# Optimization experiments

Hardware: AMD Instinct MI355X
Metric: run time of the kernel (lower is better)

## Reference

```python
import jax, jax.numpy as jnp
import numpy as np


def setup_inputs() -> dict:
    key = jax.random.key(0)
    ks = jax.random.split(key, 8)
    B, N, M, H = 8192, 2048, 2048, 10
    return {
        "X": jax.random.normal(ks[0], (B, N), dtype=jnp.float32),
        "weight": jax.random.normal(ks[1], (N, M), dtype=jnp.float32),
        "W1": jax.random.normal(ks[2], (3, H), dtype=jnp.float32) * 0.5,
        "b1": jax.random.normal(ks[3], (H,), dtype=jnp.float32) * 0.1,
        "W2": jax.random.normal(ks[4], (H, H), dtype=jnp.float32) * 0.3,
        "b2": jax.random.normal(ks[5], (H,), dtype=jnp.float32) * 0.1,
        "W3": jax.random.normal(ks[6], (H, 1), dtype=jnp.float32) * 0.3,
        "b3": jax.random.normal(ks[7], (1,), dtype=jnp.float32) * 0.1,
    }


def reference(X, weight, W1, b1, W2, b2, W3, b3):
    # NCA local rule, vectorized over all (i, j) cells.
    # 'forward'  = mean of column j excluding row i  (leave-one-out col mean)
    # 'backward' = mean of row i excluding column j  (leave-one-out row mean)
    n, m = weight.shape
    col_sum = jnp.sum(weight, axis=0, keepdims=True)            # [1, m]
    row_sum = jnp.sum(weight, axis=1, keepdims=True)            # [n, 1]
    fwd_mean = (col_sum - weight) / jnp.float32(n - 1)          # [n, m]
    bwd_mean = (row_sum - weight) / jnp.float32(m - 1)          # [n, m]
    feats = jnp.stack([weight, fwd_mean, bwd_mean], axis=-1)    # [n, m, 3]
    # tiny 3 -> 10 -> 10 -> 1 MLP applied per cell
    h = jax.nn.relu(feats @ W1 + b1)                            # [n, m, 10]
    h = jax.nn.relu(h @ W2 + b2)                                # [n, m, 10]
    updates = (h @ W3 + b3)[..., 0]                             # [n, m]
    new_weight = weight + updates
    # forward: softmax(X @ W)
    return jax.nn.softmax(X @ new_weight, axis=-1)
```

## Files before the change

### kernel.cpp

```cpp
#include <hip/hip_runtime.h>
#include <hip/hip_bf16.h>


typedef int int4v __attribute__((ext_vector_type(4)));
typedef int int16v __attribute__((ext_vector_type(16)));

#define GK 2048
#define NROWS 2048
#define MCOLS 2048
#define NCHUNK 16

#define CS_BLOCKS 128
#define RS_BLOCKS 2048
__global__ __launch_bounds__(256) void pre_kernel(
    const float* __restrict__ X, const float* __restrict__ W,
    signed char* __restrict__ X1, signed char* __restrict__ X2,
    float* __restrict__ sx1,
    float* __restrict__ part, float* __restrict__ rowS) {
  const int bid = blockIdx.x;
  const int tid = threadIdx.x;

  if (bid < CS_BLOCKS) {
    int chunk = bid >> 3;
    int j = (bid & 7) * 256 + tid;
    int i0 = chunk * (NROWS / NCHUNK);
    float s = 0.f;
    for (int i = i0; i < i0 + NROWS / NCHUNK; ++i) s += W[(size_t)i * MCOLS + j];
    part[(size_t)chunk * MCOLS + j] = s;
    return;
  }
  if (bid < CS_BLOCKS + RS_BLOCKS) {
    int row = bid - CS_BLOCKS;
    const float4* p = (const float4*)(W + (size_t)row * MCOLS);
    float4 a = p[tid];
    float4 b = p[tid + 256];
    float v = (a.x + a.y) + (a.z + a.w) + (b.x + b.y) + (b.z + b.w);
    __shared__ float red[256];
    red[tid] = v;
    __syncthreads();
    for (int s = 128; s > 0; s >>= 1) {
      if (tid < s) red[tid] += red[tid + s];
      __syncthreads();
    }
    if (tid == 0) rowS[row] = red[0];
    return;
  }
  {
    int row = bid - CS_BLOCKS - RS_BLOCKS;
    const float4* xr = (const float4*)(X + (size_t)row * GK);
    float4 a = xr[tid * 2];
    float4 b = xr[tid * 2 + 1];
    float xs[8] = {a.x, a.y, a.z, a.w, b.x, b.y, b.z, b.w};
    float am = 0.f;
#pragma unroll
    for (int i = 0; i < 8; ++i) am = fmaxf(am, fabsf(xs[i]));
    const int lane = tid & 63, wv = tid >> 6;
#pragma unroll
    for (int off = 32; off > 0; off >>= 1)
      am = fmaxf(am, __shfl_xor(am, off));
    __shared__ float wred[4];
    if (lane == 0) wred[wv] = am;
    __syncthreads();
    float amax = fmaxf(fmaxf(wred[0], wred[1]), fmaxf(wred[2], wred[3]));
    float s1 = amax * (1.0f / 127.0f);
    float inv = 127.0f / amax;
    int q1[8], q2[8];
#pragma unroll
    for (int i = 0; i < 8; ++i) {
      q1[i] = (int)rintf(xs[i] * inv);
      float r = xs[i] - (float)q1[i] * s1;
      q2[i] = (int)rintf(r * (254.0f * inv));
    }
    unsigned lo1 = (q1[0] & 255) | ((q1[1] & 255) << 8) | ((q1[2] & 255) << 16) | ((q1[3] & 255) << 24);
    unsigned hi1 = (q1[4] & 255) | ((q1[5] & 255) << 8) | ((q1[6] & 255) << 16) | ((q1[7] & 255) << 24);
    unsigned lo2 = (q2[0] & 255) | ((q2[1] & 255) << 8) | ((q2[2] & 255) << 16) | ((q2[3] & 255) << 24);
    unsigned hi2 = (q2[4] & 255) | ((q2[5] & 255) << 8) | ((q2[6] & 255) << 16) | ((q2[7] & 255) << 24);
    ((uint2*)(X1 + (size_t)row * GK))[tid] = make_uint2(lo1, hi1);
    ((uint2*)(X2 + (size_t)row * GK))[tid] = make_uint2(lo2, hi2);
    if (tid == 0) sx1[row] = s1;
  }
}

__global__ __launch_bounds__(256) void nca_update_kernel(
    const float* __restrict__ W, const float* __restrict__ part,
    const float* __restrict__ rowS,
    const float* __restrict__ W1, const float* __restrict__ b1,
    const float* __restrict__ W2, const float* __restrict__ b2,
    const float* __restrict__ W3, const float* __restrict__ b3,
    float* __restrict__ Wt) {
  __shared__ float sW1[30], sb1[10], sW2[100], sb2[10], sW3[10], sb3;
  __shared__ float sColS[32];
  __shared__ float cred[NCHUNK][33];
  __shared__ float Tf[32][33];
  const int tid = threadIdx.x;
  const int i0 = blockIdx.y * 32;
  const int j0 = blockIdx.x * 32;

  if (tid < 30) sW1[tid] = W1[tid];
  if (tid < 10) { sb1[tid] = b1[tid]; sb2[tid] = b2[tid]; sW3[tid] = W3[tid]; }
  if (tid >= 32 && tid < 132) sW2[tid - 32] = W2[tid - 32];
  if (tid == 0) sb3 = b3[0];

  {
    int ch = tid >> 5;
    int jl = tid & 31;
    cred[ch][jl]     = part[(size_t)ch * MCOLS + j0 + jl];
    cred[ch + 8][jl] = part[(size_t)(ch + 8) * MCOLS + j0 + jl];
  }
  __syncthreads();
  if (tid < 32) {
    float s = 0.f;
#pragma unroll
    for (int c = 0; c < NCHUNK; ++c) s += cred[c][tid];
    sColS[tid] = s;
  }
  __syncthreads();

  const int r = tid >> 5;
  const int c = tid & 31;

  float w[4], fwd[4], bwd[4];
#pragma unroll
  for (int cell = 0; cell < 4; ++cell) {
    int il = r + 8 * cell;
    float wv = W[(size_t)(i0 + il) * MCOLS + j0 + c];
    w[cell] = wv;
    fwd[cell] = (sColS[c] - wv) * (1.0f / (float)(NROWS - 1));
    bwd[cell] = (rowS[i0 + il] - wv) * (1.0f / (float)(MCOLS - 1));
  }

  float h1[4][10];
#pragma unroll
  for (int o = 0; o < 10; ++o) {
    float w1a = sW1[o], w1b = sW1[10 + o], w1c = sW1[20 + o], bb = sb1[o];
#pragma unroll
    for (int cell = 0; cell < 4; ++cell) {
      float v = fmaf(w[cell], w1a, fmaf(fwd[cell], w1b, fmaf(bwd[cell], w1c, bb)));
      h1[cell][o] = fmaxf(v, 0.f);
    }
  }
  float u[4] = {sb3, sb3, sb3, sb3};
#pragma unroll
  for (int o = 0; o < 10; ++o) {
    float h2[4];
    float bb = sb2[o];
#pragma unroll
    for (int cell = 0; cell < 4; ++cell) h2[cell] = bb;
#pragma unroll
    for (int p = 0; p < 10; ++p) {
      float wv = sW2[p * 10 + o];
#pragma unroll
      for (int cell = 0; cell < 4; ++cell) h2[cell] = fmaf(h1[cell][p], wv, h2[cell]);
    }
    float w3 = sW3[o];
#pragma unroll
    for (int cell = 0; cell < 4; ++cell) u[cell] = fmaf(fmaxf(h2[cell], 0.f), w3, u[cell]);
  }

#pragma unroll
  for (int cell = 0; cell < 4; ++cell) {
    int il = r + 8 * cell;
    Tf[il][c] = w[cell] + u[cell];
  }
  __syncthreads();

  {
    int r2 = tid >> 4;
    int ic = (tid & 15) * 2;
#pragma unroll
    for (int half = 0; half < 2; ++half) {
      int jl = r2 + 16 * half;
      float2 v = make_float2(Tf[ic][jl], Tf[ic + 1][jl]);
      *(float2*)(&Wt[(size_t)(j0 + jl) * NROWS + i0 + ic]) = v;
    }
  }
}

__global__ __launch_bounds__(256) void bquant_kernel(
    const float* __restrict__ Wt, signed char* __restrict__ B1,
    signed char* __restrict__ B2, float* __restrict__ sw1) {
  const int row = blockIdx.x;
  const int tid = threadIdx.x;
  const float4* wr = (const float4*)(Wt + (size_t)row * GK);
  float4 a = wr[tid * 2];
  float4 b = wr[tid * 2 + 1];
  float xs[8] = {a.x, a.y, a.z, a.w, b.x, b.y, b.z, b.w};
  float am = 0.f;
#pragma unroll
  for (int i = 0; i < 8; ++i) am = fmaxf(am, fabsf(xs[i]));
  const int lane = tid & 63, wv = tid >> 6;
#pragma unroll
  for (int off = 32; off > 0; off >>= 1)
    am = fmaxf(am, __shfl_xor(am, off));
  __shared__ float wred[4];
  if (lane == 0) wred[wv] = am;
  __syncthreads();
  float amax = fmaxf(fmaxf(wred[0], wred[1]), fmaxf(wred[2], wred[3]));
  float s1 = amax * (1.0f / 127.0f);
  float inv = 127.0f / amax;
  int q1[8], q2[8];
#pragma unroll
  for (int i = 0; i < 8; ++i) {
    q1[i] = (int)rintf(xs[i] * inv);
    float r = xs[i] - (float)q1[i] * s1;
    q2[i] = (int)rintf(r * (254.0f * inv));
  }
  unsigned lo1 = (q1[0] & 255) | ((q1[1] & 255) << 8) | ((q1[2] & 255) << 16) | ((q1[3] & 255) << 24);
  unsigned hi1 = (q1[4] & 255) | ((q1[5] & 255) << 8) | ((q1[6] & 255) << 16) | ((q1[7] & 255) << 24);
  unsigned lo2 = (q2[0] & 255) | ((q2[1] & 255) << 8) | ((q2[2] & 255) << 16) | ((q2[3] & 255) << 24);
  unsigned hi2 = (q2[4] & 255) | ((q2[5] & 255) << 8) | ((q2[6] & 255) << 16) | ((q2[7] & 255) << 24);
  ((uint2*)(B1 + (size_t)row * GK))[tid] = make_uint2(lo1, hi1);
  ((uint2*)(B2 + (size_t)row * GK))[tid] = make_uint2(lo2, hi2);
  if (tid == 0) sw1[row] = s1;
}

#define BM 256
#define BN 128
#define BK 64
#define NT (GK / BK)
#define BUFSZ 49152

__device__ __forceinline__ void glds16(const signed char* g, char* l) {
  __builtin_amdgcn_global_load_lds(
      (const __attribute__((address_space(1))) void*)g,
      (__attribute__((address_space(3))) void*)l, 16, 0, 0);
}

#define QUAD(mi, ni)                                                           \
  {                                                                            \
    acc_h[mi][ni] = __builtin_amdgcn_mfma_i32_32x32x32_i8(                     \
        a1f[mi][0], b1f[ni][0], acc_h[mi][ni], 0, 0, 0);                       \
    acc_c[mi][ni] = __builtin_amdgcn_mfma_i32_32x32x32_i8(                     \
        a1f[mi][0], b2f[ni][0], acc_c[mi][ni], 0, 0, 0);                       \
    acc_c[mi][ni] = __builtin_amdgcn_mfma_i32_32x32x32_i8(                     \
        a2f[mi][0], b1f[ni][0], acc_c[mi][ni], 0, 0, 0);                       \
    acc_h[mi][ni] = __builtin_amdgcn_mfma_i32_32x32x32_i8(                     \
        a1f[mi][1], b1f[ni][1], acc_h[mi][ni], 0, 0, 0);                       \
    acc_c[mi][ni] = __builtin_amdgcn_mfma_i32_32x32x32_i8(                     \
        a1f[mi][1], b2f[ni][1], acc_c[mi][ni], 0, 0, 0);                       \
    acc_c[mi][ni] = __builtin_amdgcn_mfma_i32_32x32x32_i8(                     \
        a2f[mi][1], b1f[ni][1], acc_c[mi][ni], 0, 0, 0);                       \
  }

__global__ __launch_bounds__(512, 2) void gemm_kernel(
    const signed char* __restrict__ X1, const signed char* __restrict__ X2,
    const signed char* __restrict__ B1, const signed char* __restrict__ B2,
    const float* __restrict__ sw1, float* __restrict__ C) {
  __shared__ __align__(16) char sL[3 * BUFSZ];

  const int tid = threadIdx.x;
  const int lane = tid & 63;
  const int wave = tid >> 6;
  const int wr = wave >> 1;
  const int wc = wave & 1;

  const int bx = blockIdx.x;
  const int by = blockIdx.y;

  const signed char* A1g = X1 + (size_t)(by * BM) * GK;
  const signed char* A2g = X2 + (size_t)(by * BM) * GK;
  const signed char* B1g = B1 + (size_t)(bx * BN) * GK;
  const signed char* B2g = B2 + (size_t)(bx * BN) * GK;

  const int srow = lane >> 2;
  const int schk = (lane & 3) ^ ((lane >> 3) & 3);
  const size_t qoff = (size_t)(wave * 16 + srow) * GK + schk * 16;
  const int wds = wave * 1024;

  const int rl = lane & 15;
  const int bhalf = (lane >> 4) & 1;
  const int kck = lane >> 5;
  int aoff[2][2], boff[2][2];
#pragma unroll
  for (int mi = 0; mi < 2; ++mi)
#pragma unroll
    for (int ks = 0; ks < 2; ++ks) {
      int c = 2 * ks + kck;
      int slot = 4 * rl + (c ^ ((rl >> 1) & 3));
      aoff[mi][ks] = (wr * 4 + mi * 2 + bhalf) * 1024 + slot * 16;
      boff[mi][ks] = 32768 + (wc * 4 + mi * 2 + bhalf) * 1024 + slot * 16;
    }

  int16v acc_h[2][2], acc_c[2][2];
#pragma unroll
  for (int i = 0; i < 2; ++i)
#pragma unroll
    for (int j = 0; j < 2; ++j)
#pragma unroll
      for (int e = 0; e < 16; ++e) { acc_h[i][j][e] = 0; acc_c[i][j][e] = 0; }

#pragma unroll
  for (int t = 0; t < 2; ++t) {
    char* wb = sL + t * BUFSZ;
    const size_t k0 = (size_t)t * BK;
    glds16(A1g + qoff + k0, wb + wds);
    glds16(A1g + qoff + (size_t)128 * GK + k0, wb + 8192 + wds);
    glds16(A2g + qoff + k0, wb + 16384 + wds);
    glds16(A2g + qoff + (size_t)128 * GK + k0, wb + 24576 + wds);
    glds16(B1g + qoff + k0, wb + 32768 + wds);
    glds16(B2g + qoff + k0, wb + 40960 + wds);
  }

  const char* sbuf = sL;
  char* wbuf = sL + 2 * BUFSZ;

  int4v a1f[2][2], a2f[2][2], b1f[2][2], b2f[2][2];

#pragma unroll 1
  for (int kt = 0; kt < NT; ++kt) {
    if (kt + 1 < NT) asm volatile("s_waitcnt vmcnt(6)" ::: "memory");
    else             asm volatile("s_waitcnt vmcnt(0)" ::: "memory");
    __builtin_amdgcn_s_barrier();
    asm volatile("" ::: "memory");

    const size_t k2 = (size_t)(kt + 2) * BK;
    const bool pf = (kt + 2 < NT);

#pragma unroll
    for (int ks = 0; ks < 2; ++ks) {
      a1f[0][ks] = *(const int4v*)(sbuf + aoff[0][ks]);
      a2f[0][ks] = *(const int4v*)(sbuf + aoff[0][ks] + 16384);
      b1f[0][ks] = *(const int4v*)(sbuf + boff[0][ks]);
      b2f[0][ks] = *(const int4v*)(sbuf + boff[0][ks] + 8192);
    }
    if (pf) {
      glds16(A1g + qoff + k2, wbuf + wds);
      glds16(A1g + qoff + (size_t)128 * GK + k2, wbuf + 8192 + wds);
    }
#pragma unroll
    for (int ks = 0; ks < 2; ++ks) {
      b1f[1][ks] = *(const int4v*)(sbuf + boff[1][ks]);
      b2f[1][ks] = *(const int4v*)(sbuf + boff[1][ks] + 8192);
    }
    if (pf) {
      glds16(A2g + qoff + k2, wbuf + 16384 + wds);
      glds16(A2g + qoff + (size_t)128 * GK + k2, wbuf + 24576 + wds);
    }
#pragma unroll
    for (int ks = 0; ks < 2; ++ks) {
      a1f[1][ks] = *(const int4v*)(sbuf + aoff[1][ks]);
      a2f[1][ks] = *(const int4v*)(sbuf + aoff[1][ks] + 16384);
    }
    if (pf) {
      glds16(B1g + qoff + k2, wbuf + 32768 + wds);
      glds16(B2g + qoff + k2, wbuf + 40960 + wds);
    }

    __builtin_amdgcn_s_setprio(1);
    QUAD(0, 0);
    QUAD(0, 1);
    QUAD(1, 1);
    QUAD(1, 0);
    __builtin_amdgcn_s_setprio(0);

    sbuf += BUFSZ; if (sbuf == sL + 3 * BUFSZ) sbuf = sL;
    wbuf += BUFSZ; if (wbuf == sL + 3 * BUFSZ) wbuf = sL;
  }

  const int ecol = lane & 31;
  const int erow = 4 * (lane >> 5);
#pragma unroll
  for (int ni = 0; ni < 2; ++ni) {
    int col = bx * BN + wc * 64 + ni * 32 + ecol;
    float sw = sw1[col];
#pragma unroll
    for (int mi = 0; mi < 2; ++mi) {
#pragma unroll
      for (int reg = 0; reg < 16; ++reg) {
        int row = by * BM + wr * 64 + mi * 32 + (reg & 3) + 8 * (reg >> 2) + erow;
        float v = (float)acc_h[mi][ni][reg] + (float)acc_c[mi][ni][reg] * (1.0f / 254.0f);
        C[(size_t)row * MCOLS + col] = v * sw;
      }
    }
  }
}

__global__ __launch_bounds__(256) void softmax_kernel(
    float* __restrict__ C, const float* __restrict__ sx1) {
  const int lane = threadIdx.x & 63;
  const int wv = threadIdx.x >> 6;
  const int row = blockIdx.x * 4 + wv;
  const float sx = sx1[row];
  float4* p = (float4*)(C + (size_t)row * MCOLS);

  float4 v[8];
#pragma unroll
  for (int j = 0; j < 8; ++j) {
    v[j] = p[j * 64 + lane];
    v[j].x *= sx; v[j].y *= sx; v[j].z *= sx; v[j].w *= sx;
  }

  float vmax = -3.4e38f;
#pragma unroll
  for (int j = 0; j < 8; ++j)
    vmax = fmaxf(vmax, fmaxf(fmaxf(v[j].x, v[j].y), fmaxf(v[j].z, v[j].w)));
#pragma unroll
  for (int off = 32; off > 0; off >>= 1)
    vmax = fmaxf(vmax, __shfl_xor(vmax, off));

  float sum = 0.f;
#pragma unroll
  for (int j = 0; j < 8; ++j) {
    v[j].x = __expf(v[j].x - vmax);
    v[j].y = __expf(v[j].y - vmax);
    v[j].z = __expf(v[j].z - vmax);
    v[j].w = __expf(v[j].w - vmax);
    sum += (v[j].x + v[j].y) + (v[j].z + v[j].w);
  }
#pragma unroll
  for (int off = 32; off > 0; off >>= 1)
    sum += __shfl_xor(sum, off);
  float inv = 1.0f / sum;

#pragma unroll
  for (int j = 0; j < 8; ++j) {
    v[j].x *= inv; v[j].y *= inv; v[j].z *= inv; v[j].w *= inv;
    p[j * 64 + lane] = v[j];
  }
}

extern "C" void kernel_launch(void* const* d_in, const int* in_sizes, int n_in,
                              void* d_out, int out_size, void* d_ws, size_t ws_size,
                              hipStream_t stream) {
  const float* X      = (const float*)d_in[0];
  const float* weight = (const float*)d_in[1];
  const float* W1     = (const float*)d_in[2];
  const float* b1     = (const float*)d_in[3];
  const float* W2     = (const float*)d_in[4];
  const float* b2     = (const float*)d_in[5];
  const float* W3     = (const float*)d_in[6];
  const float* b3     = (const float*)d_in[7];
  float* out = (float*)d_out;

  const int N = 2048, M = 2048;
  const int Bdim = in_sizes[0] / N;

  float* rowS = (float*)d_ws;
  float* part = rowS + 2048;
  float* sx1  = part + NCHUNK * 2048;
  float* sw1  = sx1 + 8192;
  float* Wt   = sw1 + 2048;
  signed char* X1 = (signed char*)(Wt + (size_t)M * N);
  signed char* X2 = X1 + (size_t)Bdim * N;
  signed char* B1q = X2 + (size_t)Bdim * N;
  signed char* B2q = B1q + (size_t)M * N;

  pre_kernel<<<CS_BLOCKS + RS_BLOCKS + Bdim, 256, 0, stream>>>(
      X, weight, X1, X2, sx1, part, rowS);

  nca_update_kernel<<<dim3(M / 32, N / 32), 256, 0, stream>>>(
      weight, part, rowS, W1, b1, W2, b2, W3, b3, Wt);

  bquant_kernel<<<M, 256, 0, stream>>>(Wt, B1q, B2q, sw1);

  gemm_kernel<<<dim3(M / BN, Bdim / BM), 512, 0, stream>>>(
      X1, X2, B1q, B2q, sw1, out);

  softmax_kernel<<<Bdim / 4, 256, 0, stream>>>(out, sx1);
}
```

Measured before the change: 297.4 us.

## Split MFMA block into halves gated by explicit LDS waitcnts to overlap reads

Replaces the compiler-generated LDS fragment loads with inline-asm ds_read_b128 and reorders them so all B fragments and the first A row load first. Waits with lgkmcnt(4) and runs the first half of the MFMAs (mi=0) while the mi=1 A fragments are still in flight, then waits for the rest before the second half. Sched barriers pin this order. The aim is to hide LDS read latency behind matrix work. The risk is that hand-placed waitcnts have to match the exact instruction count, since inline asm hides these loads from the compiler's dependency tracking.

```diff
diff --git a/kernel.cpp b/kernel.cpp
--- a/kernel.cpp
+++ b/kernel.cpp
@@ -226,20 +226,40 @@
       (__attribute__((address_space(3))) void*)l, 16, 0, 0);
 }
 
-#define QUAD(mi, ni)                                                           \
+__device__ __forceinline__ int4v ds_read128(const char* p) {
+  int4v r;
+  asm volatile("ds_read_b128 %0, %1"
+               : "=v"(r)
+               : "v"((const __attribute__((address_space(3))) char*)p));
+  return r;
+}
+
+#define PAIR(mi)                                                               \
   {                                                                            \
-    acc_h[mi][ni] = __builtin_amdgcn_mfma_i32_32x32x32_i8(                     \
-        a1f[mi][0], b1f[ni][0], acc_h[mi][ni], 0, 0, 0);                       \
-    acc_c[mi][ni] = __builtin_amdgcn_mfma_i32_32x32x32_i8(                     \
-        a1f[mi][0], b2f[ni][0], acc_c[mi][ni], 0, 0, 0);                       \
-    acc_c[mi][ni] = __builtin_amdgcn_mfma_i32_32x32x32_i8(                     \
-        a2f[mi][0], b1f[ni][0], acc_c[mi][ni], 0, 0, 0);                       \
-    acc_h[mi][ni] = __builtin_amdgcn_mfma_i32_32x32x32_i8(                     \
-        a1f[mi][1], b1f[ni][1], acc_h[mi][ni], 0, 0, 0);                       \
-    acc_c[mi][ni] = __builtin_amdgcn_mfma_i32_32x32x32_i8(                     \
-        a1f[mi][1], b2f[ni][1], acc_c[mi][ni], 0, 0, 0);                       \
-    acc_c[mi][ni] = __builtin_amdgcn_mfma_i32_32x32x32_i8(                     \
-        a2f[mi][1], b1f[ni][1], acc_c[mi][ni], 0, 0, 0);                       \
+    acc_h[mi][0] = __builtin_amdgcn_mfma_i32_32x32x32_i8(                      \
+        a1f[mi][0], b1f[0][0], acc_h[mi][0], 0, 0, 0);                         \
+    acc_h[mi][1] = __builtin_amdgcn_mfma_i32_32x32x32_i8(                      \
+        a1f[mi][0], b1f[1][0], acc_h[mi][1], 0, 0, 0);                         \
+    acc_c[mi][0] = __builtin_amdgcn_mfma_i32_32x32x32_i8(                      \
+        a1f[mi][0], b2f[0][0], acc_c[mi][0], 0, 0, 0);                         \
+    acc_c[mi][1] = __builtin_amdgcn_mfma_i32_32x32x32_i8(                      \
+        a1f[mi][0], b2f[1][0], acc_c[mi][1], 0, 0, 0);                         \
+    acc_c[mi][0] = __builtin_amdgcn_mfma_i32_32x32x32_i8(                      \
+        a2f[mi][0], b1f[0][0], acc_c[mi][0], 0, 0, 0);                         \
+    acc_c[mi][1] = __builtin_amdgcn_mfma_i32_32x32x32_i8(                      \
+        a2f[mi][0], b1f[1][0], acc_c[mi][1], 0, 0, 0);                         \
+    acc_h[mi][0] = __builtin_amdgcn_mfma_i32_32x32x32_i8(                      \
+        a1f[mi][1], b1f[0][1], acc_h[mi][0], 0, 0, 0);                         \
+    acc_h[mi][1] = __builtin_amdgcn_mfma_i32_32x32x32_i8(                      \
+        a1f[mi][1], b1f[1][1], acc_h[mi][1], 0, 0, 0);                         \
+    acc_c[mi][0] = __builtin_amdgcn_mfma_i32_32x32x32_i8(                      \
+        a1f[mi][1], b2f[0][1], acc_c[mi][0], 0, 0, 0);                         \
+    acc_c[mi][1] = __builtin_amdgcn_mfma_i32_32x32x32_i8(                      \
+        a1f[mi][1], b2f[1][1], acc_c[mi][1], 0, 0, 0);                         \
+    acc_c[mi][0] = __builtin_amdgcn_mfma_i32_32x32x32_i8(                      \
+        a2f[mi][1], b1f[0][1], acc_c[mi][0], 0, 0, 0);                         \
+    acc_c[mi][1] = __builtin_amdgcn_mfma_i32_32x32x32_i8(                      \
+        a2f[mi][1], b1f[1][1], acc_c[mi][1], 0, 0, 0);                         \
   }
 
 __global__ __launch_bounds__(512, 2) void gemm_kernel(
@@ -311,46 +331,47 @@
     if (kt + 1 < NT) asm volatile("s_waitcnt vmcnt(6)" ::: "memory");
     else             asm volatile("s_waitcnt vmcnt(0)" ::: "memory");
     __builtin_amdgcn_s_barrier();
-    asm volatile("" ::: "memory");
 
     const size_t k2 = (size_t)(kt + 2) * BK;
     const bool pf = (kt + 2 < NT);
 
 #pragma unroll
+    for (int ni = 0; ni < 2; ++ni)
+#pragma unroll
+      for (int ks = 0; ks < 2; ++ks) {
+        b1f[ni][ks] = ds_read128(sbuf + boff[ni][ks]);
+        b2f[ni][ks] = ds_read128(sbuf + boff[ni][ks] + 8192);
+      }
+#pragma unroll
     for (int ks = 0; ks < 2; ++ks) {
-      a1f[0][ks] = *(const int4v*)(sbuf + aoff[0][ks]);
-      a2f[0][ks] = *(const int4v*)(sbuf + aoff[0][ks] + 16384);
-      b1f[0][ks] = *(const int4v*)(sbuf + boff[0][ks]);
-      b2f[0][ks] = *(const int4v*)(sbuf + boff[0][ks] + 8192);
+      a1f[0][ks] = ds_read128(sbuf + aoff[0][ks]);
+      a2f[0][ks] = ds_read128(sbuf + aoff[0][ks] + 16384);
     }
     if (pf) {
       glds16(A1g + qoff + k2, wbuf + wds);
       glds16(A1g + qoff + (size_t)128 * GK + k2, wbuf + 8192 + wds);
+      glds16(A2g + qoff + k2, wbuf + 16384 + wds);
     }
 #pragma unroll
     for (int ks = 0; ks < 2; ++ks) {
-      b1f[1][ks] = *(const int4v*)(sbuf + boff[1][ks]);
-      b2f[1][ks] = *(const int4v*)(sbuf + boff[1][ks] + 8192);
+      a1f[1][ks] = ds_read128(sbuf + aoff[1][ks]);
+      a2f[1][ks] = ds_read128(sbuf + aoff[1][ks] + 16384);
     }
     if (pf) {
-      glds16(A2g + qoff + k2, wbuf + 16384 + wds);
       glds16(A2g + qoff + (size_t)128 * GK + k2, wbuf + 24576 + wds);
-    }
-#pragma unroll
-    for (int ks = 0; ks < 2; ++ks) {
-      a1f[1][ks] = *(const int4v*)(sbuf + aoff[1][ks]);
-      a2f[1][ks] = *(const int4v*)(sbuf + aoff[1][ks] + 16384);
-    }
-    if (pf) {
       glds16(B1g + qoff + k2, wbuf + 32768 + wds);
       glds16(B2g + qoff + k2, wbuf + 40960 + wds);
     }
 
+    asm volatile("s_waitcnt lgkmcnt(4)" ::: "memory");
+    __builtin_amdgcn_sched_barrier(0);
     __builtin_amdgcn_s_setprio(1);
-    QUAD(0, 0);
-    QUAD(0, 1);
-    QUAD(1, 1);
-    QUAD(1, 0);
+    PAIR(0);
+    __builtin_amdgcn_s_setprio(0);
+    asm volatile("s_waitcnt lgkmcnt(0)" ::: "memory");
+    __builtin_amdgcn_sched_barrier(0);
+    __builtin_amdgcn_s_setprio(1);
+    PAIR(1);
     __builtin_amdgcn_s_setprio(0);
 
     sbuf += BUFSZ; if (sbuf == sL + 3 * BUFSZ) sbuf = sL;
```

After: 290.5 us. 2.3% less time.
